# Optimization experiments

Measured on AMD Instinct MI355X. Metric: run time of the kernel, lower is better.

Reference implementation:

```python
import jax, jax.numpy as jnp
import numpy as np

N, F, E = 2048, 4, 65536
D, H, FF = 256, 4, 2048  # d_model, n_heads, transformer feedforward dim
HD = D // H


def setup_inputs() -> dict:
    key = jax.random.key(0)
    ks = jax.random.split(key, 26)
    p = lambda k, shape, fan_in: (jax.random.normal(k, shape, jnp.float32) / np.sqrt(fan_in))
    return {
        "features": jax.random.normal(ks[0], (N, F), jnp.float32),
        "edges": jax.random.randint(ks[1], (2, E), 0, N, jnp.int64),
        # Embedder.linear: Linear(1, 256)
        "lin_w": p(ks[2], (D, 1), 1), "lin_b": jnp.zeros((D,), jnp.float32),
        # TransformerEncoderLayer self-attention
        "in_proj_w": p(ks[3], (3 * D, D), D), "in_proj_b": jnp.zeros((3 * D,), jnp.float32),
        "out_w": p(ks[4], (D, D), D), "out_b": jnp.zeros((D,), jnp.float32),
        "ln1_g": jnp.ones((D,), jnp.float32), "ln1_b": jnp.zeros((D,), jnp.float32),
        # feedforward
        "ffn_w1": p(ks[5], (FF, D), D), "ffn_b1": jnp.zeros((FF,), jnp.float32),
        "ffn_w2": p(ks[6], (D, FF), FF), "ffn_b2": jnp.zeros((D,), jnp.float32),
        "ln2_g": jnp.ones((D,), jnp.float32), "ln2_b": jnp.zeros((D,), jnp.float32),
        # 4 GCNConv layers (torch Linear convention: weight [out, in])
        "W1": p(ks[7], (512, D), D), "b1": jnp.zeros((512,), jnp.float32),
        "W2": p(ks[8], (512, 512), 512), "b2": jnp.zeros((512,), jnp.float32),
        "W3": p(ks[9], (512, 512), 512), "b3": jnp.zeros((512,), jnp.float32),
        "W4": p(ks[10], (512, 512), 512), "b4": jnp.zeros((512,), jnp.float32),
    }


def _layer_norm(x, g, b, eps=1e-5):
    m = jnp.mean(x, axis=-1, keepdims=True)
    v = jnp.mean((x - m) ** 2, axis=-1, keepdims=True)
    return (x - m) / jnp.sqrt(v + eps) * g + b


def _gcn_conv(x, W, b, src, dst, n):
    # PyG GCNConv: h = x @ W^T; add self-loops; norm = deg^-1/2[src]*deg^-1/2[dst];
    # out = scatter_add(norm * h[src] -> dst) + bias
    h = x @ W.T
    loop = jnp.arange(n, dtype=src.dtype)
    s = jnp.concatenate([src, loop])
    d = jnp.concatenate([dst, loop])
    deg = jax.ops.segment_sum(jnp.ones_like(d, dtype=h.dtype), d, num_segments=n)
    dinv = jnp.where(deg > 0, deg ** -0.5, 0.0)
    norm = dinv[s] * dinv[d]
    return jax.ops.segment_sum(h[s] * norm[:, None], d, num_segments=n) + b


def reference(features, edges, lin_w, lin_b, in_proj_w, in_proj_b, out_w, out_b,
              ln1_g, ln1_b, ffn_w1, ffn_b1, ffn_w2, ffn_b2, ln2_g, ln2_b,
              W1, b1, W2, b2, W3, b3, W4, b4):
    n, f = features.shape
    # Embedder: [N,F,1] -> Linear(1,D) -> [N,F,D]; seq-first transformer (seq=N, batch=F)
    x = features[..., None] @ lin_w.T + lin_b  # [N,F,D]
    qkv = x @ in_proj_w.T + in_proj_b          # [N,F,3D]
    q, k, v = jnp.split(qkv, 3, axis=-1)
    split = lambda t: t.reshape(n, f, H, HD).transpose(1, 2, 0, 3)  # [F,H,N,hd]
    q, k, v = split(q), split(k), split(v)
    scores = jnp.einsum('bhqd,bhkd->bhqk', q, k) / np.sqrt(HD)      # [F,H,N,N]
    attn = jax.nn.softmax(scores, axis=-1)
    o = jnp.einsum('bhqk,bhkd->bhqd', attn, v).transpose(2, 0, 1, 3).reshape(n, f, D)
    o = o @ out_w.T + out_b
    x = _layer_norm(x + o, ln1_g, ln1_b)
    ff = jax.nn.relu(x @ ffn_w1.T + ffn_b1) @ ffn_w2.T + ffn_b2
    x = _layer_norm(x + ff, ln2_g, ln2_b)
    x = jax.nn.relu(jnp.mean(x, axis=1))  # mean over feature-batch dim -> [N,D]

    src, dst = edges[0], edges[1]
    x = jax.nn.relu(_gcn_conv(x, W1, b1, src, dst, n))
    x = jax.nn.relu(_gcn_conv(x, W2, b2, src, dst, n))
    x = jax.nn.relu(_gcn_conv(x, W3, b3, src, dst, n))
    x = _gcn_conv(x, W4, b4, src, dst, n)
    return x
```

## Files before the change

kernel.cpp:

```cpp
#include <hip/hip_runtime.h>
#include <hip/hip_bf16.h>
#include <math.h>

#define NN   2048
#define FB   4
#define DD   256
#define EE   65536
#define NT   (NN*FB)
#define FFD  2048

typedef unsigned int u32;
typedef unsigned short u16;
typedef __attribute__((ext_vector_type(4))) float f32x4;
typedef __attribute__((ext_vector_type(8))) short bf16x8;

#define OFF_W2   0
#define OFF_G1   524288
#define OFF_G2   655360
#define OFF_G3   917504
#define OFF_G4   1179648
#define WBF_TOT  1441792

__device__ float g_A[768], g_B[768];
__device__ float g_coefA[4], g_coefC[4];
__device__ float g_meanv[6], g_G[36];
__device__ float g_Vx[8*DD];
__device__ u16   g_w1vh[FFD*8];
__device__ float g_m[NT*4];
__device__ float g_cc[NT*8];
__device__ u16   g_xmh[NN*DD];
__device__ u16   g_hsh[NN*512];
__device__ u16   g_xgh[NN*512];
__device__ u16   g_wbf[WBF_TOT];
__device__ __align__(64) int g_degp[NN*16];
__device__ __align__(64) int g_curp[NN*16];
__device__ int   g_off[NN+1], g_adj[EE];
__device__ float g_dinv[NN];

__device__ __forceinline__ u16 f2bf(float x) {
  u32 u = __float_as_uint(x);
  return (u16)((u + 0x7FFFu + ((u >> 16) & 1u)) >> 16);
}
__device__ __forceinline__ float bfl(u32 v) { return __uint_as_float(v << 16); }
__device__ __forceinline__ float bfh(u32 v) { return __uint_as_float(v & 0xffff0000u); }
__device__ __forceinline__ void gl_lds16(const void* g, void* l) {
  __builtin_amdgcn_global_load_lds(
      (const __attribute__((address_space(1))) u32*)g,
      (__attribute__((address_space(3))) u32*)l, 16, 0, 0);
}
__device__ __forceinline__ float qred(float v) {
  v += __shfl_xor(v, 1, 64);
  v += __shfl_xor(v, 2, 64);
  return v;
}
__device__ __forceinline__ void acc8(const uint4 v, float* a) {
  a[0]+=bfl(v.x); a[1]+=bfh(v.x);
  a[2]+=bfl(v.y); a[3]+=bfh(v.y);
  a[4]+=bfl(v.z); a[5]+=bfh(v.z);
  a[6]+=bfl(v.w); a[7]+=bfh(v.w);
}

__global__ __launch_bounds__(256) void k_fuse1(const float* __restrict__ ipw,
    const float* __restrict__ ipb, const float* __restrict__ linw,
    const float* __restrict__ linb) {
  __shared__ __align__(16) float sm[512];
  const int b = blockIdx.x, t = threadIdx.x;
  if (b < 12) {
    float* lw = sm; float* lb = sm + 256;
    lw[t] = linw[t]; lb[t] = linb[t];
    __syncthreads();
    int j = b*64 + (t>>2), c = t&3;
    const float4* row = (const float4*)&ipw[j*256 + c*64];
    float a = 0.f, bb = 0.f;
    #pragma unroll
    for (int q = 0; q < 16; q++) {
      float4 v = row[q]; int d0 = c*64 + q*4;
      a  += v.x*lw[d0] + v.y*lw[d0+1] + v.z*lw[d0+2] + v.w*lw[d0+3];
      bb += v.x*lb[d0] + v.y*lb[d0+1] + v.z*lb[d0+2] + v.w*lb[d0+3];
    }
    a = qred(a); bb = qred(bb);
    if (c == 0) { g_A[j] = a; g_B[j] = bb + ipb[j]; }
  } else {
    int i = (b - 12)*256 + t;
    if (i < NN*16) { g_degp[i] = 0; g_curp[i] = 0; }
  }
}

__global__ __launch_bounds__(256) void k_fuse2(const float* __restrict__ outw,
    const float* __restrict__ outb, const float* __restrict__ linw,
    const float* __restrict__ linb, const float* __restrict__ g1,
    const float* __restrict__ b1ln, const int* __restrict__ edges) {
  __shared__ __align__(16) float sm[512 + 4*27];
  const int b = blockIdx.x, t = threadIdx.x;
  if (b == 0) {
    int lane = t & 63, w = t >> 6;
    {
      float aq = g_A[w*64 + lane], ak = g_A[256 + w*64 + lane], bq = g_B[w*64 + lane];
      float pa = aq * ak, pc = bq * ak;
      #pragma unroll
      for (int o = 32; o > 0; o >>= 1) { pa += __shfl_down(pa, o, 64); pc += __shfl_down(pc, o, 64); }
      if (lane == 0) { g_coefA[w] = pa * 0.125f; g_coefC[w] = pc * 0.125f; }
    }
    float* A2 = sm; float* B2 = sm + 256; float* wred = sm + 512;
    A2[t] = g_A[512 + t]; B2[t] = g_B[512 + t];
    __syncthreads();
    const int d = t;
    const float4* row = (const float4*)&outw[d*256];
    float pv[4] = {0,0,0,0}, q0 = 0.f;
    #pragma unroll 8
    for (int q = 0; q < 64; q++) {
      float4 v = row[q]; int e0 = q*4; int h = q >> 4;
      pv[h] += v.x*A2[e0] + v.y*A2[e0+1] + v.z*A2[e0+2] + v.w*A2[e0+3];
      q0    += v.x*B2[e0] + v.y*B2[e0+1] + v.z*B2[e0+2] + v.w*B2[e0+3];
    }
    q0 += outb[d];
    float c0 = linb[d] + q0;
    float Mv[6] = { linw[d], pv[0], pv[1], pv[2], pv[3], c0 };
    float vals[27];
    { int idx = 0;
      #pragma unroll
      for (int k = 0; k < 6; k++) vals[idx++] = Mv[k];
      #pragma unroll
      for (int k = 0; k < 6; k++)
        #pragma unroll
        for (int l = 0; l < 6; l++) if (l >= k) vals[idx++] = Mv[k]*Mv[l];
    }
    #pragma unroll
    for (int k2 = 0; k2 < 27; k2++) {
      float v = vals[k2];
      #pragma unroll
      for (int o = 32; o > 0; o >>= 1) v += __shfl_down(v, o, 64);
      if (lane == 0) wred[w*27 + k2] = v;
    }
    __syncthreads();
    if (t < 27) {
      float s = wred[t] + wred[27 + t] + wred[54 + t] + wred[81 + t];
      if (t < 6) g_meanv[t] = s * (1.f/256.f);
      else {
        int p = t - 6, k = 0;
        while (p >= 6 - k) { p -= 6 - k; k++; }
        int l = k + p;
        g_G[k*6+l] = s; g_G[l*6+k] = s;
      }
    }
    #pragma unroll
    for (int k = 0; k < 6; k++) g_Vx[k*256 + d] = Mv[k] * g1[d];
    g_Vx[6*256 + d] = g1[d];
    g_Vx[7*256 + d] = b1ln[d];
  } else {
    int e = (b - 1)*256 + t;
    atomicAdd(&g_degp[edges[EE + e] * 16], 1);
  }
}

__global__ __launch_bounds__(256) void k_fuse3(const float* __restrict__ feat,
    const float* __restrict__ w1, const float* __restrict__ fb1,
    const float* __restrict__ w2c, const float* __restrict__ W1c,
    const float* __restrict__ W2c, const float* __restrict__ W3c,
    const float* __restrict__ W4c) {
  __shared__ __align__(16) char smraw[34816];
  const int b = blockIdx.x, t = threadIdx.x;
  if (b < 512) {
    float* fs = (float*)smraw;
    float* ss = fs + 8192;
    float* ww = ss + 256;
    for (int i = t; i < 2048; i += 256) {
      const float4 v = *(const float4*)&feat[i*4];
      fs[0*2048+i] = v.x; fs[1*2048+i] = v.y; fs[2*2048+i] = v.z; fs[3*2048+i] = v.w;
    }
    __syncthreads();
    int tuple = b * 64 + (t >> 2);
    int c = t & 3;
    int h = tuple & 3, f = (tuple >> 2) & 3, n = tuple >> 4;
    float fi = fs[f*2048 + n];
    float tt = g_coefA[h] * fi + g_coefC[h];
    float s = 0.f, wsum = 0.f;
    int j0 = c * 512;
    for (int j = j0; j < j0 + 512; j++) {
      float fj = fs[f*2048 + j];
      float e = __expf(tt * fj);
      s += e; wsum += e * fj;
    }
    ss[(t>>2)*4 + c] = s; ww[(t>>2)*4 + c] = wsum;
    __syncthreads();
    if (c == 0) {
      float S = ss[(t>>2)*4] + ss[(t>>2)*4+1] + ss[(t>>2)*4+2] + ss[(t>>2)*4+3];
      float W = ww[(t>>2)*4] + ww[(t>>2)*4+1] + ww[(t>>2)*4+2] + ww[(t>>2)*4+3];
      g_m[tuple] = W / S;
    }
  } else if (b < 544) {
    float* vx = (float*)smraw;
    #pragma unroll
    for (int k = 0; k < 8; k++) vx[k*256 + t] = g_Vx[k*256 + t];
    __syncthreads();
    int j = (b - 512)*64 + (t>>2), c = t&3;
    const float4* row = (const float4*)&w1[j*256 + c*64];
    float acc[8] = {0,0,0,0,0,0,0,0};
    #pragma unroll
    for (int q = 0; q < 16; q++) {
      float4 v = row[q]; int d0 = c*64 + q*4;
      #pragma unroll
      for (int k = 0; k < 8; k++)
        acc[k] += v.x*vx[k*256+d0] + v.y*vx[k*256+d0+1]
                + v.z*vx[k*256+d0+2] + v.w*vx[k*256+d0+3];
    }
    #pragma unroll
    for (int k = 0; k < 8; k++) acc[k] = qred(acc[k]);
    if (c == 0) {
      acc[7] += fb1[j];
      uint4 r;
      r.x = ((u32)f2bf(acc[1])<<16) | f2bf(acc[0]);
      r.y = ((u32)f2bf(acc[3])<<16) | f2bf(acc[2]);
      r.z = ((u32)f2bf(acc[5])<<16) | f2bf(acc[4]);
      r.w = ((u32)f2bf(acc[7])<<16) | f2bf(acc[6]);
      *(uint4*)&g_w1vh[j*8] = r;
    }
  } else if (b == 544) {
    int* wt = (int*)smraw;
    int base = t * 8;
    int v[8], ex[8], sum = 0;
    #pragma unroll
    for (int i = 0; i < 8; i++) { ex[i] = sum; v[i] = g_degp[(base+i)*16]; sum += v[i]; }
    int lane = t & 63, w = t >> 6;
    int inc = sum;
    #pragma unroll
    for (int o = 1; o < 64; o <<= 1) { int x = __shfl_up(inc, o, 64); if (lane >= o) inc += x; }
    if (lane == 63) wt[w] = inc;
    __syncthreads();
    int wb = 0;
    for (int j = 0; j < w; j++) wb += wt[j];
    int excl = wb + inc - sum;
    #pragma unroll
    for (int i = 0; i < 8; i++) {
      g_off[base+i] = excl + ex[i];
      g_dinv[base+i] = rsqrtf((float)(v[i] + 1));
    }
    if (t == 255) g_off[NN] = wb + inc;
  } else {
    int i = ((b - 545)*256 + t) * 4;
    const float* src; int off;
    if (i < OFF_G1)      { src = w2c; off = OFF_W2; }
    else if (i < OFF_G2) { src = W1c; off = OFF_G1; }
    else if (i < OFF_G3) { src = W2c; off = OFF_G2; }
    else if (i < OFF_G4) { src = W3c; off = OFF_G3; }
    else                 { src = W4c; off = OFF_G4; }
    float4 v = *(const float4*)&src[i - off];
    ushort4 r;
    r.x = f2bf(v.x); r.y = f2bf(v.y); r.z = f2bf(v.z); r.w = f2bf(v.w);
    *(ushort4*)&g_wbf[i] = r;
  }
}

__global__ __launch_bounds__(256) void k_fuse4(const float* __restrict__ feat) {
  const int b = blockIdx.x, t = threadIdx.x;
  int tok = b * 256 + t;
  int n = tok >> 2, f = tok & 3;
  float fi = feat[n*4 + f];
  float u[6] = { fi, g_m[tok*4+0], g_m[tok*4+1], g_m[tok*4+2], g_m[tok*4+3], 1.f };
  float mu = 0.f;
  #pragma unroll
  for (int k = 0; k < 6; k++) mu += g_meanv[k] * u[k];
  float q = 0.f;
  for (int k = 0; k < 6; k++)
    for (int l = 0; l < 6; l++) q += u[k] * g_G[k*6+l] * u[l];
  q *= (1.f/256.f);
  float var = q - mu * mu;
  float s = rsqrtf(var + 1e-5f);
  float4 w0; w0.x = fi*s; w0.y = u[1]*s; w0.z = u[2]*s; w0.w = u[3]*s;
  float4 w1v; w1v.x = u[4]*s; w1v.y = s; w1v.z = -mu*s; w1v.w = 1.f;
  *(float4*)&g_cc[tok*8]     = w0;
  *(float4*)&g_cc[tok*8 + 4] = w1v;
}

__global__ __launch_bounds__(256) void k_ffnln(const float* __restrict__ fb2,
    const float* __restrict__ ln2g, const float* __restrict__ ln2b,
    const int* __restrict__ edges) {
  __shared__ __align__(16) char smp[74752];
  u16*   Bsl  = (u16*)smp;
  u16*   Asl  = (u16*)(smp + 65536);
  u16*   w1sl = (u16*)(smp + 69632);
  float* ccs  = (float*)(smp + 73728);
  float* part = (float*)(smp + 74240);

  const int b = blockIdx.x, t = threadIdx.x;
  if (b >= 512) {
    int e = (b - 512)*256 + t;
    int s = edges[e], d = edges[EE + e];
    int pos = atomicAdd(&g_curp[d*16], 1);
    g_adj[g_off[d] + pos] = s;
    return;
  }
  const int w = t >> 6, lane = t & 63, fr = lane & 15, gk = lane >> 4;
  const int tok0 = b * 16;
  const u16* W2p = g_wbf + OFF_W2;

  if (t < 32) ((float4*)ccs)[t] = ((const float4*)&g_cc[tok0*8])[t];
  if (w == 1) {
    #pragma unroll
    for (int hh = 0; hh < 2; hh++) {
      int p = hh*64 + lane;
      int q = (p & ~7) | ((p ^ (p >> 3)) & 7);
      gl_lds16(g_w1vh + (size_t)q*8, w1sl + (hh << 9));
    }
  }
  __syncthreads();

  const int arow = t >> 4, aslot = t & 15;
  float ac[8];
  #pragma unroll
  for (int k = 0; k < 8; k++) ac[k] = ccs[arow*8 + k];

  f32x4 acc[4] = {};
  for (int it = 0; it < 16; it++) {
    const int k0 = it << 7;
    const int cur = it & 1;
    #pragma unroll
    for (int c = 0; c < 16; c++) {
      int col0 = (w << 6) + (c << 2);
      int colL = col0 + (lane >> 4);
      int p = lane & 15;
      int q = (p & 8) | ((p ^ (colL & 7)) & 7);
      gl_lds16(W2p + (size_t)colL*FFD + k0 + q*8, Bsl + (col0 << 7));
    }
    if (w == 1 && it < 15) {
      #pragma unroll
      for (int hh = 0; hh < 2; hh++) {
        int p = hh*64 + lane;
        int q = (p & ~7) | ((p ^ (p >> 3)) & 7);
        gl_lds16(g_w1vh + (size_t)(k0 + 128 + q)*8, w1sl + ((cur ^ 1) << 10) + (hh << 9));
      }
    }
    {
      float h[8];
      #pragma unroll
      for (int e2 = 0; e2 < 8; e2++) {
        int ph = aslot*8 + (e2 ^ (aslot & 7));
        uint4 wv = *(const uint4*)&w1sl[(cur << 10) + ph*8];
        float s = ac[0]*bfl(wv.x) + ac[1]*bfh(wv.x)
                + ac[2]*bfl(wv.y) + ac[3]*bfh(wv.y)
                + ac[4]*bfl(wv.z) + ac[5]*bfh(wv.z)
                + ac[6]*bfl(wv.w) + ac[7]*bfh(wv.w);
        h[e2] = fmaxf(s, 0.f);
      }
      uint4 r;
      r.x = ((u32)f2bf(h[1])<<16) | f2bf(h[0]);
      r.y = ((u32)f2bf(h[3])<<16) | f2bf(h[2]);
      r.z = ((u32)f2bf(h[5])<<16) | f2bf(h[4]);
      r.w = ((u32)f2bf(h[7])<<16) | f2bf(h[6]);
      int ph = (aslot & 8) | ((aslot ^ (arow & 7)) & 7);
      *(uint4*)&Asl[(arow << 7) + (ph << 3)] = r;
    }
    __syncthreads();
    #pragma unroll
    for (int kk = 0; kk < 4; kk++) {
      int qa = (kk << 2) + gk;
      int pa = (qa & 8) | ((qa ^ (fr & 7)) & 7);
      bf16x8 af = *(const bf16x8*)&Asl[(fr << 7) + (pa << 3)];
      #pragma unroll
      for (int nb = 0; nb < 4; nb++) {
        int col = (w << 6) + (nb << 4) + fr;
        int pb = (qa & 8) | ((qa ^ (col & 7)) & 7);
        bf16x8 bv = *(const bf16x8*)&Bsl[(col << 7) + (pb << 3)];
        acc[nb] = __builtin_amdgcn_mfma_f32_16x16x32_bf16(af, bv, acc[nb], 0, 0, 0);
      }
    }
    __syncthreads();
  }

  #pragma unroll
  for (int nb = 0; nb < 4; nb++) {
    int col = (w << 6) + (nb << 4) + fr;
    float fb = fb2[col];
    #pragma unroll
    for (int r = 0; r < 4; r++) {
      int row = gk*4 + r;
      float x1 = 0.f;
      #pragma unroll
      for (int k = 0; k < 8; k++) x1 += ccs[row*8 + k] * g_Vx[k*256 + col];
      acc[nb][r] += fb + x1;
    }
  }
  float s1[4] = {0,0,0,0}, s2v[4] = {0,0,0,0};
  #pragma unroll
  for (int r = 0; r < 4; r++)
    #pragma unroll
    for (int nb = 0; nb < 4; nb++) {
      float v = acc[nb][r];
      s1[r] += v; s2v[r] += v*v;
    }
  #pragma unroll
  for (int o = 1; o < 16; o <<= 1) {
    #pragma unroll
    for (int r = 0; r < 4; r++) {
      s1[r]  += __shfl_xor(s1[r],  o, 64);
      s2v[r] += __shfl_xor(s2v[r], o, 64);
    }
  }
  if (fr == 0) {
    #pragma unroll
    for (int r = 0; r < 4; r++) {
      int row = gk*4 + r;
      part[(w*16 + row)*2 + 0] = s1[r];
      part[(w*16 + row)*2 + 1] = s2v[r];
    }
  }
  __syncthreads();
  float mu[4], inv[4];
  #pragma unroll
  for (int r = 0; r < 4; r++) {
    int row = gk*4 + r;
    float S1 = 0.f, S2 = 0.f;
    #pragma unroll
    for (int wv = 0; wv < 4; wv++) {
      S1 += part[(wv*16 + row)*2 + 0];
      S2 += part[(wv*16 + row)*2 + 1];
    }
    float m = S1 * (1.f/256.f);
    mu[r] = m;
    inv[r] = rsqrtf(S2 * (1.f/256.f) - m*m + 1e-5f);
  }
  const int node = b*4 + gk;
  #pragma unroll
  for (int nb = 0; nb < 4; nb++) {
    int col = (w << 6) + (nb << 4) + fr;
    float g = ln2g[col], bb = ln2b[col];
    float m = 0.f;
    #pragma unroll
    for (int r = 0; r < 4; r++)
      m += (acc[nb][r] - mu[r]) * inv[r] * g + bb;
    g_xmh[node*256 + col] = f2bf(fmaxf(m * 0.25f, 0.f));
  }
}

template<int DO_ROWSCALE, int OUT_BF16, int HAS_BIAS>
__global__ __launch_bounds__(256) void k_mm64(
    const u16* __restrict__ A, const u16* __restrict__ Bm, void* __restrict__ Cv,
    int M, int N, int K,
    const float* __restrict__ rowscale, const float* __restrict__ bias)
{
  __shared__ u16 Asl[32*128];
  __shared__ u16 Bsl[64*128];
  const int t = threadIdx.x;
  const int w = t >> 6, lane = t & 63;
  const int bm = blockIdx.y * 32, bn = blockIdx.x * 64;
  const int wr = w >> 1, wc = w & 1;
  const int fr = lane & 15;
  const int gk = lane >> 4;
  f32x4 acc[2] = {};
  for (int k0 = 0; k0 < K; k0 += 128) {
    #pragma unroll
    for (int c = 0; c < 2; c++) {
      int row0 = (w << 3) + (c << 2);
      int rowL = row0 + (lane >> 4);
      int p = lane & 15;
      int q = (p & 8) | ((p ^ (rowL & 7)) & 7);
      gl_lds16(A + (size_t)(bm + rowL)*K + k0 + q*8, Asl + (row0 << 7));
    }
    #pragma unroll
    for (int c = 0; c < 4; c++) {
      int row0 = (w << 4) + (c << 2);
      int rowL = row0 + (lane >> 4);
      int p = lane & 15;
      int q = (p & 8) | ((p ^ (rowL & 7)) & 7);
      gl_lds16(Bm + (size_t)(bn + rowL)*K + k0 + q*8, Bsl + (row0 << 7));
    }
    __syncthreads();
    #pragma unroll
    for (int kk = 0; kk < 4; kk++) {
      int qa = (kk << 2) + gk;
      int row = wr*16 + fr;
      int pa = (qa & 8) | ((qa ^ (row & 7)) & 7);
      bf16x8 af = *(const bf16x8*)&Asl[(row << 7) + (pa << 3)];
      #pragma unroll
      for (int nb = 0; nb < 2; nb++) {
        int col = wc*32 + nb*16 + fr;
        int pb = (qa & 8) | ((qa ^ (col & 7)) & 7);
        bf16x8 bv = *(const bf16x8*)&Bsl[(col << 7) + (pb << 3)];
        acc[nb] = __builtin_amdgcn_mfma_f32_16x16x32_bf16(af, bv, acc[nb], 0, 0, 0);
      }
    }
    __syncthreads();
  }
  #pragma unroll
  for (int r = 0; r < 4; r++) {
    int row = bm + wr*16 + gk*4 + r;
    float rs = DO_ROWSCALE ? rowscale[row] : 1.f;
    #pragma unroll
    for (int nb = 0; nb < 2; nb++) {
      int col = bn + wc*32 + nb*16 + fr;
      float v = acc[nb][r];
      if (HAS_BIAS) v += bias[col];
      if (DO_ROWSCALE) v *= rs;
      if (OUT_BF16) ((u16*)Cv)[(size_t)row*N + col] = f2bf(v);
      else ((float*)Cv)[(size_t)row*N + col] = v;
    }
  }
}

template<int OUT_BF16, int DO_RELU>
__global__ __launch_bounds__(256) void k_agg(const float* __restrict__ bias,
                                             void* __restrict__ outv) {
  __shared__ __align__(16) float red[2][512];
  const int t = threadIdx.x, w = t >> 6, lane = t & 63;
  const int pair = w >> 1, half = w & 1;
  const int i = blockIdx.x*2 + pair;
  const int d = lane * 8;
  const uint4* tbl = (const uint4*)g_hsh;
  float a[8] = {0,0,0,0,0,0,0,0};
  int e0 = g_off[i], e1 = g_off[i+1];
  int mid = (e0 + e1) >> 1;
  int es = half ? mid : e0;
  int ee = half ? e1 : mid;
  if (!half) acc8(tbl[i*64 + lane], a);
  int e = es;
  for (; e + 4 <= ee; e += 4) {
    int s0 = g_adj[e+0], s1 = g_adj[e+1], s2 = g_adj[e+2], s3 = g_adj[e+3];
    uint4 v0 = tbl[s0*64 + lane];
    uint4 v1 = tbl[s1*64 + lane];
    uint4 v2 = tbl[s2*64 + lane];
    uint4 v3 = tbl[s3*64 + lane];
    acc8(v0, a); acc8(v1, a); acc8(v2, a); acc8(v3, a);
  }
  for (; e < ee; e++) acc8(tbl[g_adj[e]*64 + lane], a);
  if (!half) {
    #pragma unroll
    for (int q = 0; q < 8; q++) red[pair][d + q] = a[q];
  }
  __syncthreads();
  if (half) {
    #pragma unroll
    for (int q = 0; q < 8; q++) a[q] += red[pair][d + q];
    float di = g_dinv[i];
    const float4 b0 = *(const float4*)&bias[d];
    const float4 b1 = *(const float4*)&bias[d+4];
    a[0]=di*a[0]+b0.x; a[1]=di*a[1]+b0.y; a[2]=di*a[2]+b0.z; a[3]=di*a[3]+b0.w;
    a[4]=di*a[4]+b1.x; a[5]=di*a[5]+b1.y; a[6]=di*a[6]+b1.z; a[7]=di*a[7]+b1.w;
    if (DO_RELU) {
      #pragma unroll
      for (int q = 0; q < 8; q++) a[q] = fmaxf(a[q], 0.f);
    }
    if (OUT_BF16) {
      uint4 r;
      r.x = ((u32)f2bf(a[1])<<16) | f2bf(a[0]);
      r.y = ((u32)f2bf(a[3])<<16) | f2bf(a[2]);
      r.z = ((u32)f2bf(a[5])<<16) | f2bf(a[4]);
      r.w = ((u32)f2bf(a[7])<<16) | f2bf(a[6]);
      *(uint4*)&((u16*)outv)[i*512 + d] = r;
    } else {
      float4 r0; r0.x=a[0]; r0.y=a[1]; r0.z=a[2]; r0.w=a[3];
      float4 r1; r1.x=a[4]; r1.y=a[5]; r1.z=a[6]; r1.w=a[7];
      *(float4*)&((float*)outv)[i*512 + d]     = r0;
      *(float4*)&((float*)outv)[i*512 + d + 4] = r1;
    }
  }
}

static float* symf(const void* s) { void* p = nullptr; (void)hipGetSymbolAddress(&p, s); return (float*)p; }

extern "C" void kernel_launch(void* const* d_in, const int* in_sizes, int n_in,
                              void* d_out, int out_size, void* d_ws, size_t ws_size,
                              hipStream_t stream) {
  const float* feat = (const float*)d_in[0];
  const int*   edges= (const int*)  d_in[1];
  const float* linw = (const float*)d_in[2];
  const float* linb = (const float*)d_in[3];
  const float* ipw  = (const float*)d_in[4];
  const float* ipb  = (const float*)d_in[5];
  const float* outw = (const float*)d_in[6];
  const float* outb = (const float*)d_in[7];
  const float* ln1g = (const float*)d_in[8];
  const float* ln1b = (const float*)d_in[9];
  const float* fw1  = (const float*)d_in[10];
  const float* fb1  = (const float*)d_in[11];
  const float* fw2  = (const float*)d_in[12];
  const float* fb2  = (const float*)d_in[13];
  const float* ln2g = (const float*)d_in[14];
  const float* ln2b = (const float*)d_in[15];
  const float* W1g  = (const float*)d_in[16];
  const float* b1g  = (const float*)d_in[17];
  const float* W2g  = (const float*)d_in[18];
  const float* b2g  = (const float*)d_in[19];
  const float* W3g  = (const float*)d_in[20];
  const float* b3g  = (const float*)d_in[21];
  const float* W4g  = (const float*)d_in[22];
  const float* b4g  = (const float*)d_in[23];
  float* out = (float*)d_out;

  u16*   p_xmh = (u16*)symf(HIP_SYMBOL(g_xmh));
  u16*   p_hsh = (u16*)symf(HIP_SYMBOL(g_hsh));
  u16*   p_xgh = (u16*)symf(HIP_SYMBOL(g_xgh));
  u16*   p_wbf = (u16*)symf(HIP_SYMBOL(g_wbf));
  float* p_dinv= symf(HIP_SYMBOL(g_dinv));

  k_fuse1<<<140,  256, 0, stream>>>(ipw, ipb, linw, linb);
  k_fuse2<<<257,  256, 0, stream>>>(outw, outb, linw, linb, ln1g, ln1b, edges);
  k_fuse3<<<1953, 256, 0, stream>>>(feat, fw1, fb1, fw2, W1g, W2g, W3g, W4g);
  k_fuse4<<<32,   256, 0, stream>>>(feat);

  k_ffnln<<<768, 256, 0, stream>>>(fb2, ln2g, ln2b, edges);

  k_mm64<1,1,0><<<dim3(8, 64), 256, 0, stream>>>(
      p_xmh, p_wbf + OFF_G1, p_hsh, NN, 512, 256, p_dinv, nullptr);
  k_agg<1,1><<<NN/2, 256, 0, stream>>>(b1g, p_xgh);
  k_mm64<1,1,0><<<dim3(8, 64), 256, 0, stream>>>(
      p_xgh, p_wbf + OFF_G2, p_hsh, NN, 512, 512, p_dinv, nullptr);
  k_agg<1,1><<<NN/2, 256, 0, stream>>>(b2g, p_xgh);
  k_mm64<1,1,0><<<dim3(8, 64), 256, 0, stream>>>(
      p_xgh, p_wbf + OFF_G3, p_hsh, NN, 512, 512, p_dinv, nullptr);
  k_agg<1,1><<<NN/2, 256, 0, stream>>>(b3g, p_xgh);
  k_mm64<1,1,0><<<dim3(8, 64), 256, 0, stream>>>(
      p_xgh, p_wbf + OFF_G4, p_hsh, NN, 512, 512, p_dinv, nullptr);
  k_agg<0,0><<<NN/2, 256, 0, stream>>>(b4g, out);
}
```

Measured before the change: 159.6 us.

## Double-buffer FFN kernel with 32-token tiles and register-fed first layer

```diff
diff --git a/kernel.cpp b/kernel.cpp
--- a/kernel.cpp
+++ b/kernel.cpp
@@ -275,160 +275,181 @@
 __global__ __launch_bounds__(256) void k_ffnln(const float* __restrict__ fb2,
     const float* __restrict__ ln2g, const float* __restrict__ ln2b,
     const int* __restrict__ edges) {
-  __shared__ __align__(16) char smp[74752];
+  __shared__ __align__(16) char smp[149504];
   u16*   Bsl  = (u16*)smp;
-  u16*   Asl  = (u16*)(smp + 65536);
-  u16*   w1sl = (u16*)(smp + 69632);
-  float* ccs  = (float*)(smp + 73728);
-  float* part = (float*)(smp + 74240);
+  u16*   Asl  = (u16*)(smp + 131072);
+  float* ccs  = (float*)(smp + 147456);
+  float* part = (float*)(smp + 148480);
 
   const int b = blockIdx.x, t = threadIdx.x;
-  if (b >= 512) {
-    int e = (b - 512)*256 + t;
+  if (b >= 256) {
+    int e = (b - 256)*256 + t;
     int s = edges[e], d = edges[EE + e];
     int pos = atomicAdd(&g_curp[d*16], 1);
     g_adj[g_off[d] + pos] = s;
     return;
   }
   const int w = t >> 6, lane = t & 63, fr = lane & 15, gk = lane >> 4;
-  const int tok0 = b * 16;
+  const int tok0 = b * 32;
   const u16* W2p = g_wbf + OFF_W2;
 
-  if (t < 32) ((float4*)ccs)[t] = ((const float4*)&g_cc[tok0*8])[t];
-  if (w == 1) {
-    #pragma unroll
-    for (int hh = 0; hh < 2; hh++) {
-      int p = hh*64 + lane;
-      int q = (p & ~7) | ((p ^ (p >> 3)) & 7);
-      gl_lds16(g_w1vh + (size_t)q*8, w1sl + (hh << 9));
-    }
-  }
+  if (t < 64) ((float4*)ccs)[t] = ((const float4*)&g_cc[tok0*8])[t];
   __syncthreads();
 
-  const int arow = t >> 4, aslot = t & 15;
+  const int arow = t >> 3;
+  const int sb = (t & 7) * 2;
   float ac[8];
   #pragma unroll
   for (int k = 0; k < 8; k++) ac[k] = ccs[arow*8 + k];
 
-  f32x4 acc[4] = {};
-  for (int it = 0; it < 16; it++) {
+  f32x4 acc[2][4] = {};
+
+  auto AGEN = [&](int it, int buf) {
     const int k0 = it << 7;
-    const int cur = it & 1;
+    #pragma unroll
+    for (int sj = 0; sj < 2; sj++) {
+      int s = sb + sj;
+      float h[8];
+      #pragma unroll
+      for (int e2 = 0; e2 < 8; e2++) {
+        uint4 wv = *(const uint4*)&g_w1vh[(size_t)(k0 + s*8 + e2)*8];
+        float sv = ac[0]*bfl(wv.x) + ac[1]*bfh(wv.x)
+                 + ac[2]*bfl(wv.y) + ac[3]*bfh(wv.y)
+                 + ac[4]*bfl(wv.z) + ac[5]*bfh(wv.z)
+                 + ac[6]*bfl(wv.w) + ac[7]*bfh(wv.w);
+        h[e2] = fmaxf(sv, 0.f);
+      }
+      uint4 r;
+      r.x = ((u32)f2bf(h[1])<<16) | f2bf(h[0]);
+      r.y = ((u32)f2bf(h[3])<<16) | f2bf(h[2]);
+      r.z = ((u32)f2bf(h[5])<<16) | f2bf(h[4]);
+      r.w = ((u32)f2bf(h[7])<<16) | f2bf(h[6]);
+      int ph = (s & 8) | ((s ^ (arow & 7)) & 7);
+      *(uint4*)&Asl[(buf << 12) + (arow << 7) + (ph << 3)] = r;
+    }
+  };
+  auto STAGE = [&](int it, int buf) {
+    const int k0 = it << 7;
     #pragma unroll
     for (int c = 0; c < 16; c++) {
       int col0 = (w << 6) + (c << 2);
       int colL = col0 + (lane >> 4);
       int p = lane & 15;
       int q = (p & 8) | ((p ^ (colL & 7)) & 7);
-      gl_lds16(W2p + (size_t)colL*FFD + k0 + q*8, Bsl + (col0 << 7));
-    }
-    if (w == 1 && it < 15) {
-      #pragma unroll
-      for (int hh = 0; hh < 2; hh++) {
-        int p = hh*64 + lane;
-        int q = (p & ~7) | ((p ^ (p >> 3)) & 7);
-        gl_lds16(g_w1vh + (size_t)(k0 + 128 + q)*8, w1sl + ((cur ^ 1) << 10) + (hh << 9));
-      }
-    }
-    {
-      float h[8];
-      #pragma unroll
-      for (int e2 = 0; e2 < 8; e2++) {
-        int ph = aslot*8 + (e2 ^ (aslot & 7));
-        uint4 wv = *(const uint4*)&w1sl[(cur << 10) + ph*8];
-        float s = ac[0]*bfl(wv.x) + ac[1]*bfh(wv.x)
-                + ac[2]*bfl(wv.y) + ac[3]*bfh(wv.y)
-                + ac[4]*bfl(wv.z) + ac[5]*bfh(wv.z)
-                + ac[6]*bfl(wv.w) + ac[7]*bfh(wv.w);
-        h[e2] = fmaxf(s, 0.f);
-      }
-      uint4 r;
-      r.x = ((u32)f2bf(h[1])<<16) | f2bf(h[0]);
-      r.y = ((u32)f2bf(h[3])<<16) | f2bf(h[2]);
-      r.z = ((u32)f2bf(h[5])<<16) | f2bf(h[4]);
-      r.w = ((u32)f2bf(h[7])<<16) | f2bf(h[6]);
-      int ph = (aslot & 8) | ((aslot ^ (arow & 7)) & 7);
-      *(uint4*)&Asl[(arow << 7) + (ph << 3)] = r;
-    }
-    __syncthreads();
+      gl_lds16(W2p + (size_t)colL*FFD + k0 + q*8, Bsl + (buf << 15) + (col0 << 7));
+    }
+  };
+
+  AGEN(0, 0);
+  STAGE(0, 0);
+  for (int it = 0; it < 16; ++it) {
+    const int cur = it & 1;
+    if (it < 15) {
+      AGEN(it + 1, cur ^ 1);
+      STAGE(it + 1, cur ^ 1);
+    } else {
+      asm volatile("s_waitcnt vmcnt(0)" ::: "memory");
+    }
+    asm volatile("s_waitcnt lgkmcnt(0)" ::: "memory");
+    __builtin_amdgcn_sched_barrier(0);
+    __builtin_amdgcn_s_barrier();
+    __builtin_amdgcn_sched_barrier(0);
     #pragma unroll
     for (int kk = 0; kk < 4; kk++) {
       int qa = (kk << 2) + gk;
-      int pa = (qa & 8) | ((qa ^ (fr & 7)) & 7);
-      bf16x8 af = *(const bf16x8*)&Asl[(fr << 7) + (pa << 3)];
+      #pragma unroll
+      for (int rb = 0; rb < 2; rb++) {
+        int row = rb*16 + fr;
+        int pa = (qa & 8) | ((qa ^ (row & 7)) & 7);
+        bf16x8 af = *(const bf16x8*)&Asl[(cur << 12) + (row << 7) + (pa << 3)];
+        #pragma unroll
+        for (int nb = 0; nb < 4; nb++) {
+          int col = (w << 6) + (nb << 4) + fr;
+          int pb = (qa & 8) | ((qa ^ (col & 7)) & 7);
+          bf16x8 bv = *(const bf16x8*)&Bsl[(cur << 15) + (col << 7) + (pb << 3)];
+          acc[rb][nb] = __builtin_amdgcn_mfma_f32_16x16x32_bf16(af, bv, acc[rb][nb], 0, 0, 0);
+        }
+      }
+    }
+    __builtin_amdgcn_sched_barrier(0);
+    __builtin_amdgcn_s_barrier();
+  }
+
+  #pragma unroll
+  for (int rb = 0; rb < 2; rb++)
+    #pragma unroll
+    for (int nb = 0; nb < 4; nb++) {
+      int col = (w << 6) + (nb << 4) + fr;
+      float fb = fb2[col];
+      #pragma unroll
+      for (int r = 0; r < 4; r++) {
+        int row = rb*16 + gk*4 + r;
+        float x1 = 0.f;
+        #pragma unroll
+        for (int k = 0; k < 8; k++) x1 += ccs[row*8 + k] * g_Vx[k*256 + col];
+        acc[rb][nb][r] += fb + x1;
+      }
+    }
+  float s1[2][4] = {}, s2v[2][4] = {};
+  #pragma unroll
+  for (int rb = 0; rb < 2; rb++)
+    #pragma unroll
+    for (int r = 0; r < 4; r++)
       #pragma unroll
       for (int nb = 0; nb < 4; nb++) {
-        int col = (w << 6) + (nb << 4) + fr;
-        int pb = (qa & 8) | ((qa ^ (col & 7)) & 7);
-        bf16x8 bv = *(const bf16x8*)&Bsl[(col << 7) + (pb << 3)];
-        acc[nb] = __builtin_amdgcn_mfma_f32_16x16x32_bf16(af, bv, acc[nb], 0, 0, 0);
-      }
-    }
-    __syncthreads();
-  }
-
-  #pragma unroll
-  for (int nb = 0; nb < 4; nb++) {
-    int col = (w << 6) + (nb << 4) + fr;
-    float fb = fb2[col];
+        float v = acc[rb][nb][r];
+        s1[rb][r] += v; s2v[rb][r] += v*v;
+      }
+  #pragma unroll
+  for (int o = 1; o < 16; o <<= 1) {
+    #pragma unroll
+    for (int rb = 0; rb < 2; rb++)
+      #pragma unroll
+      for (int r = 0; r < 4; r++) {
+        s1[rb][r]  += __shfl_xor(s1[rb][r],  o, 64);
+        s2v[rb][r] += __shfl_xor(s2v[rb][r], o, 64);
+      }
+  }
+  if (fr == 0) {
+    #pragma unroll
+    for (int rb = 0; rb < 2; rb++)
+      #pragma unroll
+      for (int r = 0; r < 4; r++) {
+        int row = rb*16 + gk*4 + r;
+        part[(w*32 + row)*2 + 0] = s1[rb][r];
+        part[(w*32 + row)*2 + 1] = s2v[rb][r];
+      }
+  }
+  __syncthreads();
+  float mu[2][4], inv[2][4];
+  #pragma unroll
+  for (int rb = 0; rb < 2; rb++)
     #pragma unroll
     for (int r = 0; r < 4; r++) {
-      int row = gk*4 + r;
-      float x1 = 0.f;
-      #pragma unroll
-      for (int k = 0; k < 8; k++) x1 += ccs[row*8 + k] * g_Vx[k*256 + col];
-      acc[nb][r] += fb + x1;
-    }
-  }
-  float s1[4] = {0,0,0,0}, s2v[4] = {0,0,0,0};
-  #pragma unroll
-  for (int r = 0; r < 4; r++)
+      int row = rb*16 + gk*4 + r;
+      float S1 = 0.f, S2 = 0.f;
+      #pragma unroll
+      for (int wv = 0; wv < 4; wv++) {
+        S1 += part[(wv*32 + row)*2 + 0];
+        S2 += part[(wv*32 + row)*2 + 1];
+      }
+      float m = S1 * (1.f/256.f);
+      mu[rb][r] = m;
+      inv[rb][r] = rsqrtf(S2 * (1.f/256.f) - m*m + 1e-5f);
+    }
+  #pragma unroll
+  for (int rb = 0; rb < 2; rb++) {
+    int node = b*8 + rb*4 + gk;
     #pragma unroll
     for (int nb = 0; nb < 4; nb++) {
-      float v = acc[nb][r];
-      s1[r] += v; s2v[r] += v*v;
-    }
-  #pragma unroll
-  for (int o = 1; o < 16; o <<= 1) {
-    #pragma unroll
-    for (int r = 0; r < 4; r++) {
-      s1[r]  += __shfl_xor(s1[r],  o, 64);
-      s2v[r] += __shfl_xor(s2v[r], o, 64);
-    }
-  }
-  if (fr == 0) {
-    #pragma unroll
-    for (int r = 0; r < 4; r++) {
-      int row = gk*4 + r;
-      part[(w*16 + row)*2 + 0] = s1[r];
-      part[(w*16 + row)*2 + 1] = s2v[r];
-    }
-  }
-  __syncthreads();
-  float mu[4], inv[4];
-  #pragma unroll
-  for (int r = 0; r < 4; r++) {
-    int row = gk*4 + r;
-    float S1 = 0.f, S2 = 0.f;
-    #pragma unroll
-    for (int wv = 0; wv < 4; wv++) {
-      S1 += part[(wv*16 + row)*2 + 0];
-      S2 += part[(wv*16 + row)*2 + 1];
-    }
-    float m = S1 * (1.f/256.f);
-    mu[r] = m;
-    inv[r] = rsqrtf(S2 * (1.f/256.f) - m*m + 1e-5f);
-  }
-  const int node = b*4 + gk;
-  #pragma unroll
-  for (int nb = 0; nb < 4; nb++) {
-    int col = (w << 6) + (nb << 4) + fr;
-    float g = ln2g[col], bb = ln2b[col];
-    float m = 0.f;
-    #pragma unroll
-    for (int r = 0; r < 4; r++)
-      m += (acc[nb][r] - mu[r]) * inv[r] * g + bb;
-    g_xmh[node*256 + col] = f2bf(fmaxf(m * 0.25f, 0.f));
+      int col = (w << 6) + (nb << 4) + fr;
+      float g = ln2g[col], bb = ln2b[col];
+      float m = 0.f;
+      #pragma unroll
+      for (int r = 0; r < 4; r++)
+        m += (acc[rb][nb][r] - mu[rb][r]) * inv[rb][r] * g + bb;
+      g_xmh[node*256 + col] = f2bf(fmaxf(m * 0.25f, 0.f));
+    }
   }
 }
 
@@ -597,7 +618,7 @@
   k_fuse3<<<1953, 256, 0, stream>>>(feat, fw1, fb1, fw2, W1g, W2g, W3g, W4g);
   k_fuse4<<<32,   256, 0, stream>>>(feat);
 
-  k_ffnln<<<768, 256, 0, stream>>>(fb2, ln2g, ln2b, edges);
+  k_ffnln<<<512, 256, 0, stream>>>(fb2, ln2g, ln2b, edges);
 
   k_mm64<1,1,0><<<dim3(8, 64), 256, 0, stream>>>(
       p_xmh, p_wbf + OFF_G1, p_hsh, NN, 512, 256, p_dinv, nullptr);
```

New measurement: 178.0 us. 11.5% more time.
